# Optimization experiments

Measured on AMD Instinct MI355X. Metric: run time of the kernel, lower is better.

Reference implementation:

```python
import jax, jax.numpy as jnp
import numpy as np

D = 64        # gat_output_dim == state_dim
HID = 128     # hidden_dim
ADIM = 2 * D  # action_dim (ope_dim + insert_dim)


def _mk(key, shape, scale=0.05):
    return jax.random.normal(key, shape, dtype=jnp.float32) * scale


def setup_inputs() -> dict:
    key = jax.random.key(0)
    ks = jax.random.split(key, 24)
    inp = {
        "ope_gat": jax.random.normal(ks[0], (8, 258, D), jnp.float32),
        "insert_gat": jax.random.normal(ks[1], (8, 256, D), jnp.float32),
        "h": jax.random.normal(ks[2], (8, D), jnp.float32),
        "c": jax.random.normal(ks[3], (8, D), jnp.float32),
        # LSTM (pytorch layout: gates i,f,g,o stacked -> [4D, in])
        "W_ih": _mk(ks[4], (4 * D, D)),
        "W_hh": _mk(ks[5], (4 * D, D)),
        "b_ih": _mk(ks[6], (4 * D,)),
        "b_hh": _mk(ks[7], (4 * D,)),
        # V_net: Linear(D,HID) -> Linear(HID,HID) -> LeakyReLU -> Linear(HID,1)
        "Wv0": _mk(ks[8], (HID, D)), "bv0": _mk(ks[9], (HID,)),
        "Wv1": _mk(ks[10], (HID, HID)), "bv1": _mk(ks[11], (HID,)),
        "Wv2": _mk(ks[12], (1, HID)), "bv2": _mk(ks[13], (1,)),
        # A_net: Linear(D+ADIM,HID) -> Linear(HID,HID) -> LeakyReLU -> Linear(HID,1)
        "Wa0": _mk(ks[14], (HID, D + ADIM)), "ba0": _mk(ks[15], (HID,)),
        "Wa1": _mk(ks[16], (HID, HID)), "ba1": _mk(ks[17], (HID,)),
        "Wa2": _mk(ks[18], (1, HID)), "ba2": _mk(ks[19], (1,)),
    }
    return inp


def _lrelu(x):
    return jnp.where(x >= 0, x, 0.01 * x)


def _forward(ope_gat, insert_gat, h, c,
             W_ih, W_hh, b_ih, b_hh,
             Wv0, bv0, Wv1, bv1, Wv2, bv2,
             Wa0, ba0, Wa1, ba1, Wa2, ba2):
    ope = ope_gat[:, 1:-1]                # [B, O, D]
    state = ope.mean(axis=-2)             # [B, D]

    # single-step LSTM (pytorch gate order i, f, g, o)
    gates = state @ W_ih.T + b_ih + h @ W_hh.T + b_hh  # [B, 4D]
    i_g, f_g, g_g, o_g = jnp.split(gates, 4, axis=-1)
    cn = jax.nn.sigmoid(f_g) * c + jax.nn.sigmoid(i_g) * jnp.tanh(g_g)
    hn = jax.nn.sigmoid(o_g) * jnp.tanh(cn)
    rnn_state = hn                        # [B, D]

    # V head (note: no activation after first linear -- name-overwrite bug)
    V = _lrelu((rnn_state @ Wv0.T + bv0) @ Wv1.T + bv1) @ Wv2.T + bv2  # [B, 1]

    # A head on the full (ope x insert) cross-join; ope side is detached.
    ope_d = jax.lax.stop_gradient(ope)    # [B, O, D]
    B, O, _ = ope_d.shape
    I = insert_gat.shape[1]
    # Decompose first linear over the concat [state | ope | insert] (exact math).
    Ws, Wo, Wi = Wa0[:, :D], Wa0[:, D:2 * D], Wa0[:, 2 * D:]
    h0 = (rnn_state @ Ws.T)[:, None, None, :] \
         + jnp.einsum('bod,hd->boh', ope_d, Wo)[:, :, None, :] \
         + jnp.einsum('bid,hd->bih', insert_gat, Wi)[:, None, :, :] \
         + ba0                              # [B, O, I, HID]
    h1 = _lrelu(jnp.einsum('boih,gh->boig', h0, Wa1) + ba1)
    A = (jnp.einsum('boih,h->boi', h1, Wa2[0]) + ba2[0]).reshape(B, O * I)
    return V, A, hn, cn


def reference(ope_gat, insert_gat, h, c,
              W_ih, W_hh, b_ih, b_hh,
              Wv0, bv0, Wv1, bv1, Wv2, bv2,
              Wa0, ba0, Wa1, ba1, Wa2, ba2):
    return _forward(ope_gat, insert_gat, h, c,
                    W_ih, W_hh, b_ih, b_hh,
                    Wv0, bv0, Wv1, bv1, Wv2, bv2,
                    Wa0, ba0, Wa1, ba1, Wa2, ba2)
```

## Files before the change

### kernel.cpp

```cpp
#include <hip/hip_runtime.h>
#include <hip/hip_bf16.h>
#include <math.h>

typedef unsigned short u16;

#define FB    524288
#define SOFF  26896
#define C1S   27920

__device__ __forceinline__ u16 f2b(float x) { __hip_bfloat16 b = __float2bfloat16(x); return *(u16*)&b; }
__device__ __forceinline__ void cvt8(const uint4 u, float* f) {
    f[0] = __uint_as_float(u.x << 16); f[1] = __uint_as_float(u.x & 0xFFFF0000u);
    f[2] = __uint_as_float(u.y << 16); f[3] = __uint_as_float(u.y & 0xFFFF0000u);
    f[4] = __uint_as_float(u.z << 16); f[5] = __uint_as_float(u.z & 0xFFFF0000u);
    f[6] = __uint_as_float(u.w << 16); f[7] = __uint_as_float(u.w & 0xFFFF0000u);
}
__device__ __forceinline__ float dot4(const float4 a, const float4 b) {
    return a.x*b.x + a.y*b.y + a.z*b.z + a.w*b.w;
}

__global__ __launch_bounds__(256) void k12_main(
    const float* __restrict__ ope, const float* __restrict__ ins,
    const float* __restrict__ hin, const float* __restrict__ cin,
    const float* __restrict__ W_ih, const float* __restrict__ W_hh,
    const float* __restrict__ b_ih, const float* __restrict__ b_hh,
    const float* __restrict__ Wv0, const float* __restrict__ bv0,
    const float* __restrict__ Wv1, const float* __restrict__ bv1,
    const float* __restrict__ Wv2, const float* __restrict__ bv2,
    const float* __restrict__ Wa0, const float* __restrict__ ba0,
    const float* __restrict__ Wa1, const float* __restrict__ ba1,
    const float* __restrict__ Wa2, const float* __restrict__ ba2,
    float* __restrict__ ws)
{
    __shared__ __align__(16) u16 Wa1s[128*136];
    __shared__ __align__(16) u16 Wsel[128*72];
    __shared__ __align__(16) u16 inrows[16*72];
    __shared__ __align__(16) float P[16*132];
    const int t = threadIdx.x;

    if (blockIdx.x < 256) {
        const int b = blockIdx.x >> 5;
        const int r0 = (blockIdx.x & 31) * 16;
        const int side = (r0 >= 256) ? 1 : 0;

        #pragma unroll
        for (int k = 0; k < 16; ++k) {
            const int e4 = t + k*256;
            const int g = e4 >> 5, hq = (e4 & 31) * 4;
            const float4 w = *(const float4*)(Wa1 + g*128 + hq);
            ushort4 u; u.x = f2b(w.x); u.y = f2b(w.y); u.z = f2b(w.z); u.w = f2b(w.w);
            *(ushort4*)&Wa1s[g*136 + hq] = u;
        }
        #pragma unroll
        for (int k = 0; k < 8; ++k) {
            const int e4 = t + k*256;
            const int h = e4 >> 4, dq = (e4 & 15) * 4;
            const float4 w = *(const float4*)(Wa0 + h*192 + 64 + side*64 + dq);
            ushort4 u; u.x = f2b(w.x); u.y = f2b(w.y); u.z = f2b(w.z); u.w = f2b(w.w);
            *(ushort4*)&Wsel[h*72 + dq] = u;
        }
        {
            const int r = t >> 4, dq = (t & 15) * 4;
            const float* src = side
                ? (ins + b*16384 + (r0 - 256 + r)*64 + dq)
                : (ope + b*16512 + (1 + r0 + r)*64 + dq);
            const float4 w = *(const float4*)src;
            ushort4 u; u.x = f2b(w.x); u.y = f2b(w.y); u.z = f2b(w.z); u.w = f2b(w.w);
            *(ushort4*)&inrows[r*72 + dq] = u;
        }
        __syncthreads();

        const int r = t >> 4;
        const int q = t & 15;

        {
            float acc[8] = {0.f,0.f,0.f,0.f,0.f,0.f,0.f,0.f};
            #pragma unroll
            for (int d8 = 0; d8 < 64; d8 += 8) {
                float iv[8];
                cvt8(*(const uint4*)&inrows[r*72 + d8], iv);
                #pragma unroll
                for (int k = 0; k < 8; ++k) {
                    float wv[8];
                    cvt8(*(const uint4*)&Wsel[(q + 16*k)*72 + d8], wv);
                    #pragma unroll
                    for (int j = 0; j < 8; ++j) acc[k] += wv[j] * iv[j];
                }
            }
            #pragma unroll
            for (int k = 0; k < 8; ++k) P[r*132 + q + 16*k] = acc[k];
        }
        __syncthreads();

        {
            float acc[8] = {0.f,0.f,0.f,0.f,0.f,0.f,0.f,0.f};
            #pragma unroll
            for (int h8 = 0; h8 < 128; h8 += 8) {
                const float4 p0 = *(const float4*)&P[r*132 + h8];
                const float4 p1 = *(const float4*)&P[r*132 + h8 + 4];
                #pragma unroll
                for (int k = 0; k < 8; ++k) {
                    float wv[8];
                    cvt8(*(const uint4*)&Wa1s[(q + 16*k)*136 + h8], wv);
                    float a = acc[k];
                    a += wv[0]*p0.x + wv[1]*p0.y + wv[2]*p0.z + wv[3]*p0.w;
                    a += wv[4]*p1.x + wv[5]*p1.y + wv[6]*p1.z + wv[7]*p1.w;
                    acc[k] = a;
                }
            }
            float part = 0.f;
            const int row = side ? (b*256 + r0 - 256 + r) : (b*256 + r0 + r);
            float* dst = side ? (ws + 262144 + row*128) : (ws + row*128);
            #pragma unroll
            for (int k = 0; k < 8; ++k) {
                const int g = q + 16*k;
                part = fmaf(0.505f * Wa2[g], acc[k], part);
                dst[g] = acc[k];
            }
            part += __shfl_xor(part, 1);
            part += __shfl_xor(part, 2);
            part += __shfl_xor(part, 4);
            part += __shfl_xor(part, 8);
            if (q == 0) {
                if (!side) ws[FB + 2320 + row] = part;
                else       ws[FB + 4368 + row] = part;
            }
        }
    } else {
        const int b = blockIdx.x - 256;
        float* f = (float*)Wa1s;
        float* state = f;
        float* hvec  = f + 64;
        float* gl    = f + 128;
        float* hn_s  = f + 384;
        float* t0a   = f + 448;
        float* t1a   = f + 576;
        float* s2s   = f + 704;
        float* red   = f + 832;

        {
            const int d = t & 63, q = t >> 6;
            const float* p = ope + b*16512 + (1 + q*64)*64 + d;
            float s = 0.f;
            #pragma unroll 8
            for (int r = 0; r < 64; ++r) s += p[r*64];
            red[t] = s;
        }
        __syncthreads();
        if (t < 64)       state[t]   = (red[t] + red[t+64] + red[t+128] + red[t+192]) * (1.f/256.f);
        else if (t < 128) hvec[t-64] = hin[b*64 + (t-64)];
        __syncthreads();

        {
            float g = b_ih[t] + b_hh[t];
            const float4* wi = (const float4*)(W_ih + t*64);
            const float4* wh = (const float4*)(W_hh + t*64);
            #pragma unroll
            for (int k = 0; k < 16; ++k)
                g += dot4(wi[k], *(const float4*)&state[k*4])
                   + dot4(wh[k], *(const float4*)&hvec[k*4]);
            gl[t] = g;
        }
        __syncthreads();

        if (t < 64) {
            const float ig = gl[t], fg = gl[64+t], gg = gl[128+t], og = gl[192+t];
            const float c  = cin[b*64 + t];
            const float si = 1.f/(1.f + expf(-ig));
            const float sf = 1.f/(1.f + expf(-fg));
            const float so = 1.f/(1.f + expf(-og));
            const float cn = sf*c + si*tanhf(gg);
            const float hn = so*tanhf(cn);
            ws[FB + 1288 + b*64 + t] = hn;
            ws[FB + 1800 + b*64 + t] = cn;
            hn_s[t] = hn;
        }
        __syncthreads();

        if (t < 128) {
            float a = bv0[t];
            const float4* w = (const float4*)(Wv0 + t*64);
            #pragma unroll
            for (int k = 0; k < 16; ++k) a += dot4(w[k], *(const float4*)&hn_s[k*4]);
            t0a[t] = a;
        }
        __syncthreads();
        if (t < 128) {
            float a = bv1[t];
            const float4* w = (const float4*)(Wv1 + t*128);
            #pragma unroll
            for (int k = 0; k < 32; ++k) a += dot4(w[k], *(const float4*)&t0a[k*4]);
            a = (a >= 0.f) ? a : 0.01f*a;
            t1a[t] = a * Wv2[t];
            float s2 = ba0[t];
            const float4* w0 = (const float4*)(Wa0 + t*192);
            #pragma unroll
            for (int k = 0; k < 16; ++k) s2 += dot4(w0[k], *(const float4*)&hn_s[k*4]);
            s2s[t] = s2;
        }
        __syncthreads();
        if (t < 128) {
            float sv = ba1[t];
            const float4* w = (const float4*)(Wa1 + t*128);
            #pragma unroll
            for (int k = 0; k < 32; ++k) sv += dot4(w[k], *(const float4*)&s2s[k*4]);
            ws[FB + SOFF + b*128 + t] = sv;
            red[t] = 0.505f * Wa2[t] * sv;
        }
        __syncthreads();
        if (t < 64) {
            float c = red[t] + red[t + 64];
            float v = t1a[t] + t1a[t + 64];
            c += __shfl_xor(c, 32); v += __shfl_xor(v, 32);
            c += __shfl_xor(c, 16); v += __shfl_xor(v, 16);
            c += __shfl_xor(c, 8);  v += __shfl_xor(v, 8);
            c += __shfl_xor(c, 4);  v += __shfl_xor(v, 4);
            c += __shfl_xor(c, 2);  v += __shfl_xor(v, 2);
            c += __shfl_xor(c, 1);  v += __shfl_xor(v, 1);
            if (t == 0) {
                ws[FB + C1S + b]  = c + ba2[0];
                ws[FB + 1280 + b] = v + bv2[0];
            }
        }
    }
}

__global__ __launch_bounds__(256) void k3_adv(const float* __restrict__ ws,
                                              const float* __restrict__ Wa2,
                                              float* __restrict__ out)
{
    const int t = threadIdx.x;
    const int b = blockIdx.x >> 6;
    const int o0 = (blockIdx.x & 63) * 4;

    float acc[4] = {0.f, 0.f, 0.f, 0.f};
    #pragma unroll
    for (int gc = 0; gc < 8; ++gc) {
        float syv[16], wv[16];
        {
            const float* yr = ws + 262144 + (b*256 + t)*128 + gc*16;
            const float* sr = ws + FB + SOFF + b*128 + gc*16;
            const float* wr = Wa2 + gc*16;
            #pragma unroll
            for (int k = 0; k < 4; ++k) {
                const float4 y4 = *(const float4*)(yr + k*4);
                const float4 s4 = *(const float4*)(sr + k*4);
                const float4 w4 = *(const float4*)(wr + k*4);
                syv[k*4+0] = y4.x + s4.x; syv[k*4+1] = y4.y + s4.y;
                syv[k*4+2] = y4.z + s4.z; syv[k*4+3] = y4.w + s4.w;
                wv[k*4+0] = 0.495f*w4.x; wv[k*4+1] = 0.495f*w4.y;
                wv[k*4+2] = 0.495f*w4.z; wv[k*4+3] = 0.495f*w4.w;
            }
        }
        #pragma unroll
        for (int o = 0; o < 4; ++o) {
            const float* xr = ws + (b*256 + o0 + o)*128 + gc*16;
            float a = acc[o];
            #pragma unroll
            for (int k = 0; k < 4; ++k) {
                const float4 x4 = *(const float4*)(xr + k*4);
                a = fmaf(wv[k*4+0], fabsf(x4.x + syv[k*4+0]), a);
                a = fmaf(wv[k*4+1], fabsf(x4.y + syv[k*4+1]), a);
                a = fmaf(wv[k*4+2], fabsf(x4.z + syv[k*4+2]), a);
                a = fmaf(wv[k*4+3], fabsf(x4.w + syv[k*4+3]), a);
            }
            acc[o] = a;
        }
    }
    const float c2  = ws[FB + 4368 + b*256 + t];
    const float c1s = ws[FB + C1S + b];
    #pragma unroll
    for (int o = 0; o < 4; ++o)
        out[8 + b*65536 + (o0 + o)*256 + t] =
            ws[FB + 2320 + b*256 + o0 + o] + c1s + c2 + acc[o];

    if (blockIdx.x == 0) {
        if (t < 8) out[t] = ws[FB + 1280 + t];
        #pragma unroll
        for (int j = t; j < 512; j += 256) {
            out[524296 + j] = ws[FB + 1288 + j];
            out[524808 + j] = ws[FB + 1800 + j];
        }
    }
}

extern "C" void kernel_launch(void* const* d_in, const int* in_sizes, int n_in,
                              void* d_out, int out_size, void* d_ws, size_t ws_size,
                              hipStream_t stream) {
    float* ws = (float*)d_ws;
    float* out = (float*)d_out;

    k12_main<<<dim3(264), dim3(256), 0, stream>>>(
        (const float*)d_in[0], (const float*)d_in[1],
        (const float*)d_in[2], (const float*)d_in[3],
        (const float*)d_in[4], (const float*)d_in[5],
        (const float*)d_in[6], (const float*)d_in[7],
        (const float*)d_in[8], (const float*)d_in[9],
        (const float*)d_in[10], (const float*)d_in[11],
        (const float*)d_in[12], (const float*)d_in[13],
        (const float*)d_in[14], (const float*)d_in[15],
        (const float*)d_in[16], (const float*)d_in[17],
        (const float*)d_in[18], (const float*)d_in[19], ws);
    k3_adv  <<<dim3(512), dim3(256), 0, stream>>>(ws, (const float*)d_in[18], out);
}
```

Measured before the change: 123.3 us.

## Fuse both kernels into one persistent launch with a software grid barrier

```diff
diff --git a/kernel.cpp b/kernel.cpp
--- a/kernel.cpp
+++ b/kernel.cpp
@@ -4,9 +4,13 @@
 
 typedef unsigned short u16;
 
-#define FB    524288
-#define SOFF  26896
-#define C1S   27920
+#define FB     524288
+#define SOFF   26896
+#define C1S    27920
+#define BFLAG  (FB + 28000)
+#define BCNT   (FB + 28001)
+#define MAGIC  0x5A17C0DE
+#define NBLK   264
 
 __device__ __forceinline__ u16 f2b(float x) { __hip_bfloat16 b = __float2bfloat16(x); return *(u16*)&b; }
 __device__ __forceinline__ void cvt8(const uint4 u, float* f) {
@@ -18,8 +22,11 @@
 __device__ __forceinline__ float dot4(const float4 a, const float4 b) {
     return a.x*b.x + a.y*b.y + a.z*b.z + a.w*b.w;
 }
-
-__global__ __launch_bounds__(256) void k12_main(
+__device__ __forceinline__ int aload(int* p) {
+    return __hip_atomic_load(p, __ATOMIC_ACQUIRE, __HIP_MEMORY_SCOPE_AGENT);
+}
+
+__global__ __launch_bounds__(256) void k_all(
     const float* __restrict__ ope, const float* __restrict__ ins,
     const float* __restrict__ hin, const float* __restrict__ cin,
     const float* __restrict__ W_ih, const float* __restrict__ W_hh,
@@ -30,13 +37,19 @@
     const float* __restrict__ Wa0, const float* __restrict__ ba0,
     const float* __restrict__ Wa1, const float* __restrict__ ba1,
     const float* __restrict__ Wa2, const float* __restrict__ ba2,
-    float* __restrict__ ws)
+    float* __restrict__ ws, float* __restrict__ out)
 {
     __shared__ __align__(16) u16 Wa1s[128*136];
     __shared__ __align__(16) u16 Wsel[128*72];
     __shared__ __align__(16) u16 inrows[16*72];
     __shared__ __align__(16) float P[16*132];
     const int t = threadIdx.x;
+    int* wsi = (int*)ws;
+
+    if (blockIdx.x == 0 && t == 0) {
+        __hip_atomic_store(&wsi[BCNT], 0, __ATOMIC_RELAXED, __HIP_MEMORY_SCOPE_AGENT);
+        __hip_atomic_store(&wsi[BFLAG], MAGIC, __ATOMIC_RELEASE, __HIP_MEMORY_SCOPE_AGENT);
+    }
 
     if (blockIdx.x < 256) {
         const int b = blockIdx.x >> 5;
@@ -223,56 +236,63 @@
             }
         }
     }
-}
-
-__global__ __launch_bounds__(256) void k3_adv(const float* __restrict__ ws,
-                                              const float* __restrict__ Wa2,
-                                              float* __restrict__ out)
-{
-    const int t = threadIdx.x;
-    const int b = blockIdx.x >> 6;
-    const int o0 = (blockIdx.x & 63) * 4;
-
-    float acc[4] = {0.f, 0.f, 0.f, 0.f};
-    #pragma unroll
-    for (int gc = 0; gc < 8; ++gc) {
-        float syv[16], wv[16];
-        {
-            const float* yr = ws + 262144 + (b*256 + t)*128 + gc*16;
-            const float* sr = ws + FB + SOFF + b*128 + gc*16;
-            const float* wr = Wa2 + gc*16;
-            #pragma unroll
-            for (int k = 0; k < 4; ++k) {
-                const float4 y4 = *(const float4*)(yr + k*4);
-                const float4 s4 = *(const float4*)(sr + k*4);
-                const float4 w4 = *(const float4*)(wr + k*4);
-                syv[k*4+0] = y4.x + s4.x; syv[k*4+1] = y4.y + s4.y;
-                syv[k*4+2] = y4.z + s4.z; syv[k*4+3] = y4.w + s4.w;
-                wv[k*4+0] = 0.495f*w4.x; wv[k*4+1] = 0.495f*w4.y;
-                wv[k*4+2] = 0.495f*w4.z; wv[k*4+3] = 0.495f*w4.w;
-            }
-        }
-        #pragma unroll
-        for (int o = 0; o < 4; ++o) {
-            const float* xr = ws + (b*256 + o0 + o)*128 + gc*16;
-            float a = acc[o];
-            #pragma unroll
-            for (int k = 0; k < 4; ++k) {
-                const float4 x4 = *(const float4*)(xr + k*4);
-                a = fmaf(wv[k*4+0], fabsf(x4.x + syv[k*4+0]), a);
-                a = fmaf(wv[k*4+1], fabsf(x4.y + syv[k*4+1]), a);
-                a = fmaf(wv[k*4+2], fabsf(x4.z + syv[k*4+2]), a);
-                a = fmaf(wv[k*4+3], fabsf(x4.w + syv[k*4+3]), a);
-            }
-            acc[o] = a;
-        }
-    }
-    const float c2  = ws[FB + 4368 + b*256 + t];
-    const float c1s = ws[FB + C1S + b];
-    #pragma unroll
-    for (int o = 0; o < 4; ++o)
-        out[8 + b*65536 + (o0 + o)*256 + t] =
-            ws[FB + 2320 + b*256 + o0 + o] + c1s + c2 + acc[o];
+
+    __syncthreads();
+    if (t == 0) {
+        int it = 0;
+        while (aload(&wsi[BFLAG]) != MAGIC && it < 5000000) ++it;
+        __threadfence();
+        __hip_atomic_fetch_add(&wsi[BCNT], 1, __ATOMIC_ACQ_REL, __HIP_MEMORY_SCOPE_AGENT);
+        it = 0;
+        while (aload(&wsi[BCNT]) < NBLK && it < 5000000) ++it;
+    }
+    __syncthreads();
+
+    for (int u = blockIdx.x; u < 512; u += NBLK) {
+        const int b = u >> 6;
+        const int o0 = (u & 63) * 4;
+
+        float acc[4] = {0.f, 0.f, 0.f, 0.f};
+        #pragma unroll
+        for (int gc = 0; gc < 8; ++gc) {
+            float syv[16], wv[16];
+            {
+                const float* yr = ws + 262144 + (b*256 + t)*128 + gc*16;
+                const float* sr = ws + FB + SOFF + b*128 + gc*16;
+                const float* wr = Wa2 + gc*16;
+                #pragma unroll
+                for (int k = 0; k < 4; ++k) {
+                    const float4 y4 = *(const float4*)(yr + k*4);
+                    const float4 s4 = *(const float4*)(sr + k*4);
+                    const float4 w4 = *(const float4*)(wr + k*4);
+                    syv[k*4+0] = y4.x + s4.x; syv[k*4+1] = y4.y + s4.y;
+                    syv[k*4+2] = y4.z + s4.z; syv[k*4+3] = y4.w + s4.w;
+                    wv[k*4+0] = 0.495f*w4.x; wv[k*4+1] = 0.495f*w4.y;
+                    wv[k*4+2] = 0.495f*w4.z; wv[k*4+3] = 0.495f*w4.w;
+                }
+            }
+            #pragma unroll
+            for (int o = 0; o < 4; ++o) {
+                const float* xr = ws + (b*256 + o0 + o)*128 + gc*16;
+                float a = acc[o];
+                #pragma unroll
+                for (int k = 0; k < 4; ++k) {
+                    const float4 x4 = *(const float4*)(xr + k*4);
+                    a = fmaf(wv[k*4+0], fabsf(x4.x + syv[k*4+0]), a);
+                    a = fmaf(wv[k*4+1], fabsf(x4.y + syv[k*4+1]), a);
+                    a = fmaf(wv[k*4+2], fabsf(x4.z + syv[k*4+2]), a);
+                    a = fmaf(wv[k*4+3], fabsf(x4.w + syv[k*4+3]), a);
+                }
+                acc[o] = a;
+            }
+        }
+        const float c2  = ws[FB + 4368 + b*256 + t];
+        const float c1s = ws[FB + C1S + b];
+        #pragma unroll
+        for (int o = 0; o < 4; ++o)
+            out[8 + b*65536 + (o0 + o)*256 + t] =
+                ws[FB + 2320 + b*256 + o0 + o] + c1s + c2 + acc[o];
+    }
 
     if (blockIdx.x == 0) {
         if (t < 8) out[t] = ws[FB + 1280 + t];
@@ -290,7 +310,7 @@
     float* ws = (float*)d_ws;
     float* out = (float*)d_out;
 
-    k12_main<<<dim3(264), dim3(256), 0, stream>>>(
+    k_all<<<dim3(NBLK), dim3(256), 0, stream>>>(
         (const float*)d_in[0], (const float*)d_in[1],
         (const float*)d_in[2], (const float*)d_in[3],
         (const float*)d_in[4], (const float*)d_in[5],
@@ -300,6 +320,5 @@
         (const float*)d_in[12], (const float*)d_in[13],
         (const float*)d_in[14], (const float*)d_in[15],
         (const float*)d_in[16], (const float*)d_in[17],
-        (const float*)d_in[18], (const float*)d_in[19], ws);
-    k3_adv  <<<dim3(512), dim3(256), 0, stream>>>(ws, (const float*)d_in[18], out);
-}
+        (const float*)d_in[18], (const float*)d_in[19], ws, out);
+}
```

After: 181.1 us. 46.9% more time.
